# Optimization experiments

Hardware: AMD Instinct MI355X
Metric: run time of the kernel (lower is better)

## Reference

```python
import jax, jax.numpy as jnp
import numpy as np

B, D, SEQ, P0 = 512, 512, 192, 144
P1, P2 = P0 // 3, P0 // 6  # 48, 24


def conv1d(x, w, pad=2):
    # x: [N, C, L], w: [O, C, K]; stride-1 'same' conv (no bias), like nn.Conv1d
    return jax.lax.conv_general_dilated(x, w, window_strides=(1,), padding=[(pad, pad)],
                                        dimension_numbers=('NCH', 'OIH', 'NCH'))


def _dec_layer(x, w):
    # DecoderLayer: x [B, L, C_in] -> elu(conv over channel dim) -> [B, L, C_out]
    return jax.nn.elu(jnp.transpose(conv1d(jnp.transpose(x, (0, 2, 1)), w), (0, 2, 1)))


def _chunk_merge(out, lt, w_a, w_b, step):
    # Vectorized form of the per-chunk loop: fold chunks into batch, one conv call each.
    b, p, d = out.shape
    cnt = p // step
    ya = jax.nn.elu(conv1d(out.reshape(b * cnt, step, d), w_a))   # [b*cnt, step*f, d]
    yb = jax.nn.elu(conv1d(lt.reshape(b * cnt, step, d), w_b))
    f = w_a.shape[0] // step
    return (ya + yb).reshape(b, cnt * step * f, d)


def setup_inputs() -> dict:
    key = jax.random.key(0)
    ks = jax.random.split(key, 19)
    r = lambda i, shp: jax.random.normal(ks[i], shp, dtype=jnp.float32)
    return {
        'enc_out_true': r(0, (B, SEQ // 6, D)),
        'enc_out_pred': r(1, (B, P2, D)),
        'lot0': r(2, (B, SEQ // 3, D)),
        'lot1': r(3, (B, SEQ // 6, D)),
        'lop0': r(4, (B, P1, D)),
        'lop1': r(5, (B, P2, D)),
        'w_conv_z1': r(6, (P2, SEQ // 6, 5)) * 0.05,
        'w_conv_output': r(7, (P2, P2, 5)) * 0.05,
        'w_te0': r(8, (P1, SEQ // 3, 5)) * 0.05,
        'w_te1': r(9, (P2, SEQ // 6, 5)) * 0.05,
        'w_cm0': r(10, (P1, 2 * P1, 5)) * 0.05,
        'w_cm1': r(11, (P2, 2 * P2, 5)) * 0.05,
        'w_m0': r(12, (8, 4, 5)) * 0.05,
        'w_m20': r(13, (8, 4, 5)) * 0.05,
        'w_m1': r(14, (24, 8, 5)) * 0.05,
        'w_m21': r(15, (24, 8, 5)) * 0.05,
        'w_proj': r(16, (7, D, 5)) * 0.05,
        'w_lin': r(17, (P0, P0)) * 0.05,
        'b_lin': r(18, (P0,)) * 0.05,
    }


def reference(enc_out_true, enc_out_pred, lot0, lot1, lop0, lop1,
              w_conv_z1, w_conv_output, w_te0, w_te1, w_cm0, w_cm1,
              w_m0, w_m20, w_m1, w_m21, w_proj, w_lin, b_lin):
    # enc path: conv_z1 then merge with enc_out_pred (dropout is identity at eval)
    et = conv1d(enc_out_true, w_conv_z1)                              # [B, P2, D]
    output = jax.nn.elu(conv1d(enc_out_pred + et, w_conv_output))     # [B, P2, D]

    # ---- layer_len == 1 ----
    lt = _dec_layer(jnp.transpose(lot1, (0, 2, 1)), w_te1)            # [B, D, P2]
    lt = _dec_layer(jnp.concatenate([lt, jnp.transpose(lop1, (0, 2, 1))], axis=-1), w_cm1)  # [B, D, P2]
    output = _chunk_merge(output, jnp.transpose(lt, (0, 2, 1)), w_m0, w_m20, 4)             # [B, P1, D]

    # ---- layer_len == 0 ----
    lt = _dec_layer(jnp.transpose(lot0, (0, 2, 1)), w_te0)            # [B, D, P1]
    lt = _dec_layer(jnp.concatenate([lt, jnp.transpose(lop0, (0, 2, 1))], axis=-1), w_cm0)  # [B, D, P1]
    output = _chunk_merge(output, jnp.transpose(lt, (0, 2, 1)), w_m1, w_m21, 8)             # [B, P0, D]

    # projection conv with circular padding over length P0
    x = jnp.transpose(output, (0, 2, 1))                              # [B, D, P0]
    x = jnp.pad(x, ((0, 0), (0, 0), (2, 2)), mode='wrap')
    proj = conv1d(x, w_proj, pad=0)                                   # [B, c_out, P0]
    # Linear(P0, P0) applied along the length axis
    y = jnp.einsum('bcp,op->bco', proj, w_lin) + b_lin                # [B, c_out, P0]
    return jnp.transpose(y, (0, 2, 1))                                # [B, P0, c_out]
```

## Files before the change

### kernel.cpp

```cpp
#include <hip/hip_runtime.h>
#include <hip/hip_bf16.h>


typedef _Float16 h16;
typedef _Float16 h16x8 __attribute__((ext_vector_type(8)));
typedef _Float16 h16x4 __attribute__((ext_vector_type(4)));
typedef float    f32x4 __attribute__((ext_vector_type(4)));

#define MFMA16(a,b,c) __builtin_amdgcn_mfma_f32_16x16x32_f16((a),(b),(c),0,0,0)

__device__ __forceinline__ int clampi(int x, int lo, int hi){ return x < lo ? lo : (x > hi ? hi : x); }
__device__ __forceinline__ float eluf(float v){ return v > 0.f ? v : (__expf(v) - 1.f); }

#define S40  40
#define S56  56
#define S72  72
#define S104 104
#define SO2  72

#define ROWS 80
#define RT5  5

enum {
  OFF_WZ1  = 0,
  OFF_WOUT = 5120,
  OFF_WTE1 = 10240,
  OFF_WCM1 = 15360,
  OFF_WTE0 = 25600,
  OFF_WCM0 = 40960,
  OFF_WM0  = 64000,
  OFF_WM20 = 64512,
  OFF_WM1  = 65024,
  OFF_WM21 = 67072,
  OFF_WP   = 69120,
  PACKED_TOTAL = 93696
};

__global__ void pack_weights(const float* wz1, const float* wout, const float* wte1,
    const float* wcm1, const float* wte0, const float* wcm0,
    const float* wm0, const float* wm20, const float* wm1, const float* wm21,
    const float* wproj, h16* wp)
{
  const int t = threadIdx.x;
  auto packBig = [&](const float* src, int O, int C, h16* dst, int Opad, int Cpad){
    const int n = Opad*5*Cpad;
    for (int i = t; i < n; i += blockDim.x){
      int c = i % Cpad; int k = (i / Cpad) % 5; int o = i / (Cpad*5);
      float v = (o < O && c < C) ? src[(o*C + c)*5 + k] : 0.f;
      dst[i] = (h16)v;
    }
  };
  switch (blockIdx.x){
    case 0: packBig(wz1, 24, 32, wp+OFF_WZ1, 32, 32); break;
    case 1: packBig(wout, 24, 24, wp+OFF_WOUT, 32, 32); break;
    case 2: packBig(wte1, 24, 32, wp+OFF_WTE1, 32, 32); break;
    case 3: packBig(wcm1, 24, 48, wp+OFF_WCM1, 32, 64); break;
    case 4: packBig(wte0, 48, 64, wp+OFF_WTE0, 48, 64); break;
    case 5: packBig(wcm0, 48, 96, wp+OFF_WCM0, 48, 96); break;
    case 6: {
      for (int i = t; i < 512; i += blockDim.x){
        int q = i & 31, o = i >> 5; float v = 0.f;
        if (o < 8 && q < 20){ int k = q >> 2, c = q & 3; v = wm0[(o*4 + c)*5 + k]; }
        wp[OFF_WM0 + i] = (h16)v;
      }
      for (int i = t; i < 512; i += blockDim.x){
        int q = i & 31, o = i >> 5; float v = 0.f;
        if (o < 8 && q < 20){ int k = q >> 2, c = q & 3; v = wm20[(o*4 + c)*5 + k]; }
        wp[OFF_WM20 + i] = (h16)v;
      }
    } break;
    case 7: {
      for (int i = t; i < 2048; i += blockDim.x){
        int q = i & 63, o = i >> 6; float v = 0.f;
        if (o < 24 && q < 40){ int k = q >> 3, c = q & 7; v = wm1[(o*8 + c)*5 + k]; }
        wp[OFF_WM1 + i] = (h16)v;
      }
      for (int i = t; i < 2048; i += blockDim.x){
        int q = i & 63, o = i >> 6; float v = 0.f;
        if (o < 24 && q < 40){ int k = q >> 3, c = q & 7; v = wm21[(o*8 + c)*5 + k]; }
        wp[OFF_WM21 + i] = (h16)v;
      }
    } break;
    case 8: {
      for (int i = t; i < 48*512; i += blockDim.x){
        int d = i & 511, r = i >> 9; float v = 0.f;
        if (r < 35){ int jj = r / 5, k = r - jj*5; v = wproj[(jj*512 + d)*5 + k]; }
        wp[OFF_WP + i] = (h16)v;
      }
    } break;
  }
}


__device__ __forceinline__ void loadT(const float* __restrict__ src, int C, int CB16,
    h16* __restrict__ XT, int S, int co, int d0, int wave, int lane)
{
  const int m = lane & 15, q = lane >> 4;
  const int UNITS = CB16*RT5;
  for (int u = wave; u < UNITS; u += 8){
    const int cb = u / RT5, db = u - cb*RT5;
    const int row = db*16 + m;
    const int dg = d0 - 8 + row;
    const bool dok = ((unsigned)dg < 512u);
    const int cbase = cb*16 + q*4;
    h16x4 pk;
    #pragma unroll
    for (int i = 0; i < 4; ++i){
      const int c = cbase + i;
      float v = (dok && c < C) ? src[c*512 + dg] : 0.f;
      pk[i] = (h16)v;
    }
    *(h16x4*)(XT + row*S + co + cbase) = pk;
  }
}

__device__ __forceinline__ void zeroCols(h16* XT, int S, int c0, int nc, int tid){
  for (int i = tid; i < ROWS*nc; i += 512){
    const int r = i / nc, c = i - r*nc;
    XT[r*S + c0 + c] = (h16)0.f;
  }
}

template<int CB, int EPI>
__device__ __forceinline__ void convGemm(const h16* __restrict__ XT, int S,
    const h16* __restrict__ Wp, h16* __restrict__ XTo, int So, int co,
    int OT, int Oreal, int d0, int wave, int lane)
{
  const int m = lane & 15, kg = lane >> 4;
  const int Cpad = CB*32;
  const int NT = OT*RT5;
  h16x8 B[5][CB];
  int otPrev = -1;
  for (int tix = wave; tix < NT; tix += 8){
    const int ot = tix / RT5, rt = tix - ot*RT5;
    if (ot != otPrev){
      otPrev = ot;
      const int o = ot*16 + m;
      const h16* wb = Wp + o*5*Cpad + kg*8;
      #pragma unroll
      for (int k = 0; k < 5; ++k)
        #pragma unroll
        for (int cb = 0; cb < CB; ++cb)
          B[k][cb] = *(const h16x8*)(wb + k*Cpad + cb*32);
    }
    f32x4 acc = {0.f,0.f,0.f,0.f};
    const int rbase = rt*16 + m - 2;
    #pragma unroll
    for (int k = 0; k < 5; ++k){
      const int r = clampi(rbase + k, 0, ROWS-1);
      const h16* ap = XT + r*S + kg*8;
      #pragma unroll
      for (int cb = 0; cb < CB; ++cb)
        acc = MFMA16(*(const h16x8*)(ap + cb*32), B[k][cb], acc);
    }
    const int o = ot*16 + m;
    if (o < Oreal){
      #pragma unroll
      for (int r4 = 0; r4 < 4; ++r4){
        const int row = rt*16 + kg*4 + r4;
        const bool dz = ((unsigned)(d0 - 8 + row) < 512u);
        float v = acc[r4];
        h16* p = XTo + row*So + co + o;
        if (EPI == 0) *p = dz ? (h16)((float)(*p) + v) : (h16)0.f;
        else          *p = dz ? (h16)eluf(v)           : (h16)0.f;
      }
    }
  }
}

__device__ __forceinline__ void chunk4(const h16* __restrict__ out0, const h16* __restrict__ lt1,
    const h16* __restrict__ wA, const h16* __restrict__ wB, h16* __restrict__ out1,
    int d0, int wave, int lane)
{
  const int m = lane & 15, kg = lane >> 4;
  const h16x8 bA = *(const h16x8*)(wA + m*32 + kg*8);
  const h16x8 bB = *(const h16x8*)(wB + m*32 + kg*8);
  for (int tix = wave; tix < 6*RT5; tix += 8){
    const int j = tix / RT5, rt = tix - j*RT5;
    const int rb = rt*16 + m;
    const int r0 = clampi(rb + 2*kg - 2, 0, ROWS-1);
    const int r1 = clampi(rb + 2*kg - 1, 0, ROWS-1);
    h16x4 lo = *(const h16x4*)(out0 + r0*S40 + 4*j);
    h16x4 hi = *(const h16x4*)(out0 + r1*S40 + 4*j);
    h16x8 a = __builtin_shufflevector(lo, hi, 0,1,2,3,4,5,6,7);
    f32x4 accA = {0.f,0.f,0.f,0.f};
    accA = MFMA16(a, bA, accA);
    lo = *(const h16x4*)(lt1 + r0*S40 + 4*j);
    hi = *(const h16x4*)(lt1 + r1*S40 + 4*j);
    a = __builtin_shufflevector(lo, hi, 0,1,2,3,4,5,6,7);
    f32x4 accB = {0.f,0.f,0.f,0.f};
    accB = MFMA16(a, bB, accB);
    if (m < 8){
      #pragma unroll
      for (int r4 = 0; r4 < 4; ++r4){
        const int row = rt*16 + kg*4 + r4;
        const bool dz = ((unsigned)(d0 - 8 + row) < 512u);
        out1[row*S56 + 8*j + m] = dz ? (h16)(eluf(accA[r4]) + eluf(accB[r4])) : (h16)0.f;
      }
    }
  }
}

__device__ __forceinline__ void chunk8(const h16* __restrict__ out1, const h16* __restrict__ lt0,
    const h16* __restrict__ wA, const h16* __restrict__ wB, h16* __restrict__ o2t,
    int j, int wave, int lane)
{
  const int m = lane & 15, kg = lane >> 4;
  for (int tix = wave; tix < 8; tix += 8){
    const int ot = tix >> 2, rt = tix & 3;
    const int o = ot*16 + m;
    const h16x8 bA0 = *(const h16x8*)(wA + o*64 + kg*8);
    const h16x8 bA1 = *(const h16x8*)(wA + o*64 + 32 + kg*8);
    const h16x8 bB0 = *(const h16x8*)(wB + o*64 + kg*8);
    const h16x8 bB1 = *(const h16x8*)(wB + o*64 + 32 + kg*8);
    const int rb = rt*16 + m + 8;
    const int rA0 = rb + kg - 2;
    const int rA1 = clampi(rb + kg + 2, 0, ROWS-1);
    h16x8 a0 = *(const h16x8*)(out1 + rA0*S56 + 8*j);
    h16x8 a1 = *(const h16x8*)(out1 + rA1*S56 + 8*j);
    f32x4 accA = {0.f,0.f,0.f,0.f};
    accA = MFMA16(a0, bA0, accA);
    accA = MFMA16(a1, bA1, accA);
    a0 = *(const h16x8*)(lt0 + rA0*S56 + 8*j);
    a1 = *(const h16x8*)(lt0 + rA1*S56 + 8*j);
    f32x4 accB = {0.f,0.f,0.f,0.f};
    accB = MFMA16(a0, bB0, accB);
    accB = MFMA16(a1, bB1, accB);
    h16x4 pk;
    #pragma unroll
    for (int r4 = 0; r4 < 4; ++r4)
      pk[r4] = (h16)(eluf(accA[r4]) + eluf(accB[r4]));
    *(h16x4*)(o2t + o*SO2 + rt*16 + kg*4) = pk;
  }
}

__device__ __forceinline__ void projAcc(const h16* __restrict__ WPp, const h16* __restrict__ o2t,
    float* __restrict__ PROJ, int j, int d0, int wave, int lane)
{
  const int m = lane & 15, kg = lane >> 4;
  for (int tix = wave; tix < 6; tix += 8){
    const int ct = tix & 1, rt = tix >> 1;
    f32x4 acc = {0.f,0.f,0.f,0.f};
    const h16* ap = WPp + (rt*16 + m)*512 + d0 + kg*8;
    const h16* bp = o2t + (ct*16 + m)*SO2 + kg*8;
    #pragma unroll
    for (int ks = 0; ks < 2; ++ks)
      acc = MFMA16(*(const h16x8*)(ap + ks*32), *(const h16x8*)(bp + ks*32), acc);
    const int pl = ct*16 + m;
    if (pl < 24){
      #pragma unroll
      for (int r4 = 0; r4 < 4; ++r4){
        const int rowm = rt*16 + kg*4 + r4;
        if (rowm < 35) PROJ[rowm*144 + j*24 + pl] += acc[r4];
      }
    }
  }
}

__global__ __launch_bounds__(512, 4) void decoder_fused(
    const float* __restrict__ enc_true, const float* __restrict__ enc_pred,
    const float* __restrict__ lot0, const float* __restrict__ lot1,
    const float* __restrict__ lop0, const float* __restrict__ lop1,
    const h16* __restrict__ wp, const float* __restrict__ w_lin,
    const float* __restrict__ b_lin, float* __restrict__ out)
{
  __shared__ __align__(16) char smem[79296];
  float* PROJ = (float*)smem;
  h16* B1 = (h16*)(smem + 20160);
  h16* B2 = (h16*)(smem + 36800);
  h16* B3 = (h16*)(smem + 48320);
  h16* B4 = (h16*)(smem + 54720);
  h16* B5 = (h16*)(smem + 61120);
  h16* O2a = (h16*)(smem + 70080);
  h16* O2b = (h16*)(smem + 74688);

  const int b = blockIdx.x;
  const int tid = threadIdx.x;
  const int wave = tid >> 6, lane = tid & 63;

  const float* p_true = enc_true + (size_t)b*32*512;
  const float* p_pred = enc_pred + (size_t)b*24*512;
  const float* p_lot1 = lot1 + (size_t)b*32*512;
  const float* p_lop1 = lop1 + (size_t)b*24*512;
  const float* p_lot0 = lot0 + (size_t)b*64*512;
  const float* p_lop0 = lop0 + (size_t)b*48*512;

  for (int i = tid; i < 35*144; i += 512) PROJ[i] = 0.f;
  __syncthreads();

  for (int t = 0; t < 8; ++t){
    const int d0 = t*64;

    loadT(p_true, 32, 2, B2, S40, 0, d0, wave, lane);
    loadT(p_pred, 24, 2, B1, S40, 0, d0, wave, lane);
    __syncthreads();

    convGemm<1,0>(B2, S40, wp+OFF_WZ1, B1, S40, 0, 2, 24, d0, wave, lane);
    __syncthreads();

    convGemm<1,1>(B1, S40, wp+OFF_WOUT, B3, S40, 0, 2, 24, d0, wave, lane);
    loadT(p_lot1, 32, 2, B2, S40, 0, d0, wave, lane);
    __syncthreads();

    convGemm<1,1>(B2, S40, wp+OFF_WTE1, B1, S72, 0, 2, 24, d0, wave, lane);
    loadT(p_lop1, 24, 2, B1, S72, 24, d0, wave, lane);
    zeroCols(B1, S72, 56, 8, tid);
    __syncthreads();

    convGemm<2,1>(B1, S72, wp+OFF_WCM1, B4, S40, 0, 2, 24, d0, wave, lane);
    loadT(p_lot0, 64, 4, B2, S72, 0, d0, wave, lane);
    __syncthreads();

    chunk4(B3, B4, wp+OFF_WM0, wp+OFF_WM20, B5, d0, wave, lane);
    __syncthreads();

    convGemm<2,1>(B2, S72, wp+OFF_WTE0, B1, S104, 0, 3, 48, d0, wave, lane);
    loadT(p_lop0, 48, 3, B1, S104, 48, d0, wave, lane);
    __syncthreads();

    convGemm<3,1>(B1, S104, wp+OFF_WCM0, B2, S56, 0, 3, 48, d0, wave, lane);
    __syncthreads();

    for (int j = 0; j < 6; ++j){
      h16* o2 = (j & 1) ? O2b : O2a;
      chunk8(B5, B2, wp+OFF_WM1, wp+OFF_WM21, o2, j, wave, lane);
      __syncthreads();
      projAcc(wp+OFF_WP, o2, PROJ, j, d0, wave, lane);
    }
  }
  __syncthreads();

  float* projF = (float*)B4;
  for (int i = tid; i < 7*144; i += 512){
    const int jj = i / 144, p = i - jj*144;
    float s = 0.f;
    #pragma unroll
    for (int k = 0; k < 5; ++k){
      int pp = p + k - 2; pp = (pp + 144) % 144;
      s += PROJ[(jj*5 + k)*144 + pp];
    }
    projF[i] = s;
  }
  __syncthreads();
  for (int i = tid; i < 1008; i += 512){
    const int o = i / 7, jj = i - o*7;
    float acc = b_lin[o];
    const float* wl = w_lin + o*144;
    const float* pr = (const float*)projF + jj*144;
    for (int p = 0; p < 144; ++p) acc += pr[p] * wl[p];
    out[(size_t)b*1008 + i] = acc;
  }
}

extern "C" void kernel_launch(void* const* d_in, const int* in_sizes, int n_in,
                              void* d_out, int out_size, void* d_ws, size_t ws_size,
                              hipStream_t stream)
{
  if (ws_size < (size_t)PACKED_TOTAL * sizeof(h16)) return;
  h16* wp = (h16*)d_ws;
  pack_weights<<<9, 256, 0, stream>>>(
      (const float*)d_in[6],
      (const float*)d_in[7],
      (const float*)d_in[9],
      (const float*)d_in[11],
      (const float*)d_in[8],
      (const float*)d_in[10],
      (const float*)d_in[12],
      (const float*)d_in[13],
      (const float*)d_in[14],
      (const float*)d_in[15],
      (const float*)d_in[16],
      wp);
  decoder_fused<<<512, 512, 0, stream>>>(
      (const float*)d_in[0], (const float*)d_in[1],
      (const float*)d_in[2], (const float*)d_in[3],
      (const float*)d_in[4], (const float*)d_in[5],
      wp, (const float*)d_in[17], (const float*)d_in[18],
      (float*)d_out);
}
```

Before: 734.2 us.

## Fuse enc merge via augmented identity weights, prefetch next tile, fix wave-tile mapping

Folds the enc_out_pred residual add into the first conv by appending identity columns to the packed conv_z1 weights. This removes a separate load phase and barrier. The next tile's inputs are loaded during the last conv stage, and chunk4 now runs in the same phase as the te0 conv, cutting barriers per tile. It also gives each wave a fixed output tile so weights are loaded once, splits the MFMA chain across two accumulators for ILP, and inlines chunk8 and the projection with operands hoisted out of the j loop. This reshuffles the shared-memory buffers and slightly enlarges LDS use.

```diff
diff --git a/kernel.cpp b/kernel.cpp
--- a/kernel.cpp
+++ b/kernel.cpp
@@ -22,18 +22,18 @@
 #define RT5  5
 
 enum {
-  OFF_WZ1  = 0,
-  OFF_WOUT = 5120,
-  OFF_WTE1 = 10240,
-  OFF_WCM1 = 15360,
-  OFF_WTE0 = 25600,
-  OFF_WCM0 = 40960,
-  OFF_WM0  = 64000,
-  OFF_WM20 = 64512,
-  OFF_WM1  = 65024,
-  OFF_WM21 = 67072,
-  OFF_WP   = 69120,
-  PACKED_TOTAL = 93696
+  OFF_WAUG = 0,
+  OFF_WOUT = 10240,
+  OFF_WTE1 = 15360,
+  OFF_WCM1 = 20480,
+  OFF_WTE0 = 30720,
+  OFF_WCM0 = 46080,
+  OFF_WM0  = 69120,
+  OFF_WM20 = 69632,
+  OFF_WM1  = 70144,
+  OFF_WM21 = 72192,
+  OFF_WP   = 74240,
+  PACKED_TOTAL = 98816
 };
 
 __global__ void pack_weights(const float* wz1, const float* wout, const float* wte1,
@@ -51,7 +51,17 @@
     }
   };
   switch (blockIdx.x){
-    case 0: packBig(wz1, 24, 32, wp+OFF_WZ1, 32, 32); break;
+    case 0: {
+      for (int i = t; i < 32*5*64; i += blockDim.x){
+        int c = i & 63; int k = (i >> 6) % 5; int o = i / 320;
+        float v = 0.f;
+        if (o < 24){
+          if (c < 32) v = wz1[(o*32 + c)*5 + k];
+          else if (c == 32 + o && k == 2) v = 1.f;
+        }
+        wp[OFF_WAUG + i] = (h16)v;
+      }
+    } break;
     case 1: packBig(wout, 24, 24, wp+OFF_WOUT, 32, 32); break;
     case 2: packBig(wte1, 24, 32, wp+OFF_WTE1, 32, 32); break;
     case 3: packBig(wcm1, 24, 48, wp+OFF_WCM1, 32, 64); break;
@@ -121,53 +131,51 @@
   }
 }
 
-template<int CB, int EPI>
+template<int CB, int OT, int EPI>
 __device__ __forceinline__ void convGemm(const h16* __restrict__ XT, int S,
     const h16* __restrict__ Wp, h16* __restrict__ XTo, int So, int co,
-    int OT, int Oreal, int d0, int wave, int lane)
+    int Oreal, int d0, int wave, int lane)
 {
   const int m = lane & 15, kg = lane >> 4;
   const int Cpad = CB*32;
-  const int NT = OT*RT5;
+  int ot, g, gw;
+  if (OT == 2){ ot = wave & 1; g = wave >> 1; gw = 4; }
+  else        { ot = wave % 3; g = wave / 3; gw = (ot < 2) ? 3 : 2; }
+  const int o = ot*16 + m;
+  const h16* wb = Wp + (o*5)*Cpad + kg*8;
   h16x8 B[5][CB];
-  int otPrev = -1;
-  for (int tix = wave; tix < NT; tix += 8){
-    const int ot = tix / RT5, rt = tix - ot*RT5;
-    if (ot != otPrev){
-      otPrev = ot;
-      const int o = ot*16 + m;
-      const h16* wb = Wp + o*5*Cpad + kg*8;
-      #pragma unroll
-      for (int k = 0; k < 5; ++k)
-        #pragma unroll
-        for (int cb = 0; cb < CB; ++cb)
-          B[k][cb] = *(const h16x8*)(wb + k*Cpad + cb*32);
-    }
-    f32x4 acc = {0.f,0.f,0.f,0.f};
+  #pragma unroll
+  for (int k = 0; k < 5; ++k)
+    #pragma unroll
+    for (int cb = 0; cb < CB; ++cb)
+      B[k][cb] = *(const h16x8*)(wb + k*Cpad + cb*32);
+  for (int rt = g; rt < RT5; rt += gw){
+    f32x4 acc0 = {0.f,0.f,0.f,0.f}, acc1 = {0.f,0.f,0.f,0.f};
     const int rbase = rt*16 + m - 2;
     #pragma unroll
     for (int k = 0; k < 5; ++k){
       const int r = clampi(rbase + k, 0, ROWS-1);
       const h16* ap = XT + r*S + kg*8;
       #pragma unroll
-      for (int cb = 0; cb < CB; ++cb)
-        acc = MFMA16(*(const h16x8*)(ap + cb*32), B[k][cb], acc);
-    }
-    const int o = ot*16 + m;
+      for (int cb = 0; cb < CB; ++cb){
+        if (((k*CB + cb) & 1) == 0) acc0 = MFMA16(*(const h16x8*)(ap + cb*32), B[k][cb], acc0);
+        else                        acc1 = MFMA16(*(const h16x8*)(ap + cb*32), B[k][cb], acc1);
+      }
+    }
+    const f32x4 acc = acc0 + acc1;
     if (o < Oreal){
       #pragma unroll
       for (int r4 = 0; r4 < 4; ++r4){
         const int row = rt*16 + kg*4 + r4;
         const bool dz = ((unsigned)(d0 - 8 + row) < 512u);
-        float v = acc[r4];
-        h16* p = XTo + row*So + co + o;
-        if (EPI == 0) *p = dz ? (h16)((float)(*p) + v) : (h16)0.f;
-        else          *p = dz ? (h16)eluf(v)           : (h16)0.f;
-      }
-    }
-  }
-}
-
+        const float v = acc[r4];
+        XTo[row*So + co + o] = dz ? (h16)((EPI == 1) ? eluf(v) : v) : (h16)0.f;
+      }
+    }
+  }
+}
+
+template<int SA, int SB>
 __device__ __forceinline__ void chunk4(const h16* __restrict__ out0, const h16* __restrict__ lt1,
     const h16* __restrict__ wA, const h16* __restrict__ wB, h16* __restrict__ out1,
     int d0, int wave, int lane)
@@ -180,13 +188,13 @@
     const int rb = rt*16 + m;
     const int r0 = clampi(rb + 2*kg - 2, 0, ROWS-1);
     const int r1 = clampi(rb + 2*kg - 1, 0, ROWS-1);
-    h16x4 lo = *(const h16x4*)(out0 + r0*S40 + 4*j);
-    h16x4 hi = *(const h16x4*)(out0 + r1*S40 + 4*j);
+    h16x4 lo = *(const h16x4*)(out0 + r0*SA + 4*j);
+    h16x4 hi = *(const h16x4*)(out0 + r1*SA + 4*j);
     h16x8 a = __builtin_shufflevector(lo, hi, 0,1,2,3,4,5,6,7);
     f32x4 accA = {0.f,0.f,0.f,0.f};
     accA = MFMA16(a, bA, accA);
-    lo = *(const h16x4*)(lt1 + r0*S40 + 4*j);
-    hi = *(const h16x4*)(lt1 + r1*S40 + 4*j);
+    lo = *(const h16x4*)(lt1 + r0*SB + 4*j);
+    hi = *(const h16x4*)(lt1 + r1*SB + 4*j);
     a = __builtin_shufflevector(lo, hi, 0,1,2,3,4,5,6,7);
     f32x4 accB = {0.f,0.f,0.f,0.f};
     accB = MFMA16(a, bB, accB);
@@ -201,62 +209,6 @@
   }
 }
 
-__device__ __forceinline__ void chunk8(const h16* __restrict__ out1, const h16* __restrict__ lt0,
-    const h16* __restrict__ wA, const h16* __restrict__ wB, h16* __restrict__ o2t,
-    int j, int wave, int lane)
-{
-  const int m = lane & 15, kg = lane >> 4;
-  for (int tix = wave; tix < 8; tix += 8){
-    const int ot = tix >> 2, rt = tix & 3;
-    const int o = ot*16 + m;
-    const h16x8 bA0 = *(const h16x8*)(wA + o*64 + kg*8);
-    const h16x8 bA1 = *(const h16x8*)(wA + o*64 + 32 + kg*8);
-    const h16x8 bB0 = *(const h16x8*)(wB + o*64 + kg*8);
-    const h16x8 bB1 = *(const h16x8*)(wB + o*64 + 32 + kg*8);
-    const int rb = rt*16 + m + 8;
-    const int rA0 = rb + kg - 2;
-    const int rA1 = clampi(rb + kg + 2, 0, ROWS-1);
-    h16x8 a0 = *(const h16x8*)(out1 + rA0*S56 + 8*j);
-    h16x8 a1 = *(const h16x8*)(out1 + rA1*S56 + 8*j);
-    f32x4 accA = {0.f,0.f,0.f,0.f};
-    accA = MFMA16(a0, bA0, accA);
-    accA = MFMA16(a1, bA1, accA);
-    a0 = *(const h16x8*)(lt0 + rA0*S56 + 8*j);
-    a1 = *(const h16x8*)(lt0 + rA1*S56 + 8*j);
-    f32x4 accB = {0.f,0.f,0.f,0.f};
-    accB = MFMA16(a0, bB0, accB);
-    accB = MFMA16(a1, bB1, accB);
-    h16x4 pk;
-    #pragma unroll
-    for (int r4 = 0; r4 < 4; ++r4)
-      pk[r4] = (h16)(eluf(accA[r4]) + eluf(accB[r4]));
-    *(h16x4*)(o2t + o*SO2 + rt*16 + kg*4) = pk;
-  }
-}
-
-__device__ __forceinline__ void projAcc(const h16* __restrict__ WPp, const h16* __restrict__ o2t,
-    float* __restrict__ PROJ, int j, int d0, int wave, int lane)
-{
-  const int m = lane & 15, kg = lane >> 4;
-  for (int tix = wave; tix < 6; tix += 8){
-    const int ct = tix & 1, rt = tix >> 1;
-    f32x4 acc = {0.f,0.f,0.f,0.f};
-    const h16* ap = WPp + (rt*16 + m)*512 + d0 + kg*8;
-    const h16* bp = o2t + (ct*16 + m)*SO2 + kg*8;
-    #pragma unroll
-    for (int ks = 0; ks < 2; ++ks)
-      acc = MFMA16(*(const h16x8*)(ap + ks*32), *(const h16x8*)(bp + ks*32), acc);
-    const int pl = ct*16 + m;
-    if (pl < 24){
-      #pragma unroll
-      for (int r4 = 0; r4 < 4; ++r4){
-        const int rowm = rt*16 + kg*4 + r4;
-        if (rowm < 35) PROJ[rowm*144 + j*24 + pl] += acc[r4];
-      }
-    }
-  }
-}
-
 __global__ __launch_bounds__(512, 4) void decoder_fused(
     const float* __restrict__ enc_true, const float* __restrict__ enc_pred,
     const float* __restrict__ lot0, const float* __restrict__ lot1,
@@ -264,19 +216,20 @@
     const h16* __restrict__ wp, const float* __restrict__ w_lin,
     const float* __restrict__ b_lin, float* __restrict__ out)
 {
-  __shared__ __align__(16) char smem[79296];
+  __shared__ __align__(16) char smem[81856];
   float* PROJ = (float*)smem;
-  h16* B1 = (h16*)(smem + 20160);
-  h16* B2 = (h16*)(smem + 36800);
-  h16* B3 = (h16*)(smem + 48320);
-  h16* B4 = (h16*)(smem + 54720);
-  h16* B5 = (h16*)(smem + 61120);
-  h16* O2a = (h16*)(smem + 70080);
-  h16* O2b = (h16*)(smem + 74688);
+  h16* IN = (h16*)(smem + 20160);
+  h16* A  = (h16*)(smem + 31680);
+  h16* Bb = (h16*)(smem + 38080);
+  h16* CC = (h16*)(smem + 47040);
+  h16* D  = (h16*)(smem + 63680);
+  h16* O2a = (h16*)(smem + 72640);
+  h16* O2b = (h16*)(smem + 77248);
 
   const int b = blockIdx.x;
   const int tid = threadIdx.x;
   const int wave = tid >> 6, lane = tid & 63;
+  const int m16 = lane & 15, kg4 = lane >> 4;
 
   const float* p_true = enc_true + (size_t)b*32*512;
   const float* p_pred = enc_pred + (size_t)b*24*512;
@@ -286,51 +239,96 @@
   const float* p_lop0 = lop0 + (size_t)b*48*512;
 
   for (int i = tid; i < 35*144; i += 512) PROJ[i] = 0.f;
+  loadT(p_true, 32, 2, IN, S72, 0, 0, wave, lane);
+  loadT(p_pred, 24, 2, IN, S72, 32, 0, wave, lane);
   __syncthreads();
 
   for (int t = 0; t < 8; ++t){
     const int d0 = t*64;
 
-    loadT(p_true, 32, 2, B2, S40, 0, d0, wave, lane);
-    loadT(p_pred, 24, 2, B1, S40, 0, d0, wave, lane);
-    __syncthreads();
-
-    convGemm<1,0>(B2, S40, wp+OFF_WZ1, B1, S40, 0, 2, 24, d0, wave, lane);
-    __syncthreads();
-
-    convGemm<1,1>(B1, S40, wp+OFF_WOUT, B3, S40, 0, 2, 24, d0, wave, lane);
-    loadT(p_lot1, 32, 2, B2, S40, 0, d0, wave, lane);
-    __syncthreads();
-
-    convGemm<1,1>(B2, S40, wp+OFF_WTE1, B1, S72, 0, 2, 24, d0, wave, lane);
-    loadT(p_lop1, 24, 2, B1, S72, 24, d0, wave, lane);
-    zeroCols(B1, S72, 56, 8, tid);
-    __syncthreads();
-
-    convGemm<2,1>(B1, S72, wp+OFF_WCM1, B4, S40, 0, 2, 24, d0, wave, lane);
-    loadT(p_lot0, 64, 4, B2, S72, 0, d0, wave, lane);
-    __syncthreads();
-
-    chunk4(B3, B4, wp+OFF_WM0, wp+OFF_WM20, B5, d0, wave, lane);
-    __syncthreads();
-
-    convGemm<2,1>(B2, S72, wp+OFF_WTE0, B1, S104, 0, 3, 48, d0, wave, lane);
-    loadT(p_lop0, 48, 3, B1, S104, 48, d0, wave, lane);
-    __syncthreads();
-
-    convGemm<3,1>(B1, S104, wp+OFF_WCM0, B2, S56, 0, 3, 48, d0, wave, lane);
-    __syncthreads();
-
+    convGemm<2,2,2>(IN, S72, wp+OFF_WAUG, A, S40, 0, 32, d0, wave, lane);
+    __syncthreads();
+
+    convGemm<1,2,1>(A, S40, wp+OFF_WOUT, Bb, S56, 0, 32, d0, wave, lane);
+    loadT(p_lot1, 32, 2, IN, S72, 0, d0, wave, lane);
+    __syncthreads();
+
+    convGemm<1,2,1>(IN, S72, wp+OFF_WTE1, CC, S104, 0, 24, d0, wave, lane);
+    loadT(p_lop1, 24, 2, CC, S104, 24, d0, wave, lane);
+    zeroCols(CC, S104, 56, 8, tid);
+    __syncthreads();
+
+    convGemm<2,2,1>(CC, S104, wp+OFF_WCM1, A, S40, 0, 32, d0, wave, lane);
+    loadT(p_lot0, 64, 4, IN, S72, 0, d0, wave, lane);
+    __syncthreads();
+
+    chunk4<S56,S40>(Bb, A, wp+OFF_WM0, wp+OFF_WM20, D, d0, wave, lane);
+    convGemm<2,3,1>(IN, S72, wp+OFF_WTE0, CC, S104, 0, 48, d0, wave, lane);
+    loadT(p_lop0, 48, 3, CC, S104, 48, d0, wave, lane);
+    __syncthreads();
+
+    convGemm<3,3,1>(CC, S104, wp+OFF_WCM0, Bb, S56, 0, 48, d0, wave, lane);
+    if (t < 7){
+      loadT(p_true, 32, 2, IN, S72, 0, d0 + 64, wave, lane);
+      loadT(p_pred, 24, 2, IN, S72, 32, d0 + 64, wave, lane);
+    }
+    __syncthreads();
+
+    const int o8 = (wave >> 2)*16 + m16;
+    const h16* wA8 = wp + OFF_WM1  + o8*64 + kg4*8;
+    const h16* wB8 = wp + OFF_WM21 + o8*64 + kg4*8;
+    const h16x8 bA0 = *(const h16x8*)(wA8);
+    const h16x8 bA1 = *(const h16x8*)(wA8 + 32);
+    const h16x8 bB0 = *(const h16x8*)(wB8);
+    const h16x8 bB1 = *(const h16x8*)(wB8 + 32);
+    h16x8 apf0{}, apf1{};
+    if (wave < 6){
+      const h16* ap = wp + OFF_WP + ((wave >> 1)*16 + m16)*512 + d0 + kg4*8;
+      apf0 = *(const h16x8*)(ap);
+      apf1 = *(const h16x8*)(ap + 32);
+    }
+    const int rb8 = (wave & 3)*16 + m16 + 8;
+    const int rA0 = rb8 + kg4 - 2;
+    const int rA1 = rb8 + kg4 + 2;
     for (int j = 0; j < 6; ++j){
       h16* o2 = (j & 1) ? O2b : O2a;
-      chunk8(B5, B2, wp+OFF_WM1, wp+OFF_WM21, o2, j, wave, lane);
+      {
+        h16x8 a0 = *(const h16x8*)(D + rA0*S56 + 8*j);
+        h16x8 a1 = *(const h16x8*)(D + rA1*S56 + 8*j);
+        f32x4 accA = {0.f,0.f,0.f,0.f};
+        accA = MFMA16(a0, bA0, accA);
+        accA = MFMA16(a1, bA1, accA);
+        a0 = *(const h16x8*)(Bb + rA0*S56 + 8*j);
+        a1 = *(const h16x8*)(Bb + rA1*S56 + 8*j);
+        f32x4 accB = {0.f,0.f,0.f,0.f};
+        accB = MFMA16(a0, bB0, accB);
+        accB = MFMA16(a1, bB1, accB);
+        h16x4 pk;
+        #pragma unroll
+        for (int r4 = 0; r4 < 4; ++r4)
+          pk[r4] = (h16)(eluf(accA[r4]) + eluf(accB[r4]));
+        *(h16x4*)(o2 + o8*SO2 + (wave & 3)*16 + kg4*4) = pk;
+      }
       __syncthreads();
-      projAcc(wp+OFF_WP, o2, PROJ, j, d0, wave, lane);
+      if (wave < 6){
+        f32x4 acc = {0.f,0.f,0.f,0.f};
+        const h16* bp = o2 + ((wave & 1)*16 + m16)*SO2 + kg4*8;
+        acc = MFMA16(apf0, *(const h16x8*)(bp), acc);
+        acc = MFMA16(apf1, *(const h16x8*)(bp + 32), acc);
+        const int pl = (wave & 1)*16 + m16;
+        if (pl < 24){
+          #pragma unroll
+          for (int r4 = 0; r4 < 4; ++r4){
+            const int rowm = (wave >> 1)*16 + kg4*4 + r4;
+            if (rowm < 35) PROJ[rowm*144 + j*24 + pl] += acc[r4];
+          }
+        }
+      }
     }
   }
   __syncthreads();
 
-  float* projF = (float*)B4;
+  float* projF = (float*)A;
   for (int i = tid; i < 7*144; i += 512){
     const int jj = i / 144, p = i - jj*144;
     float s = 0.f;
```

Result: slower. 1.050 ms (+43.0%).
